# Performance work log

Measured on AMD Instinct MI355X. Metric: run time of the kernel, lower is better.

The kernel has to match this reference:

```python
import jax, jax.numpy as jnp
import numpy as np

N = 50000      # nodes
E = 800000     # edges (avg degree 16)
IN = 128       # in_feats
HID = 32       # hidden_feats per head
H = 4          # num_heads
NEG_SLOPE = 0.2


def setup_inputs() -> dict:
    key = jax.random.key(0)
    ks = jax.random.split(key, 13)
    x = jax.random.normal(ks[0], (N, IN), jnp.float32)
    src = jax.random.randint(ks[1], (E,), 0, N, jnp.int32)
    dst = jax.random.randint(ks[2], (E,), 0, N, jnp.int32)

    def lin(k, fi, fo):
        return jax.random.normal(k, (fi, fo), jnp.float32) * (1.0 / np.sqrt(fi))

    # conv1: IN -> H*HID
    W1 = lin(ks[3], IN, H * HID)
    al1 = jax.random.normal(ks[4], (H, HID), jnp.float32) * 0.1
    ar1 = jax.random.normal(ks[5], (H, HID), jnp.float32) * 0.1
    b1 = jnp.zeros((H, HID), jnp.float32)
    # conv2: H*HID -> H*HID
    W2 = lin(ks[6], H * HID, H * HID)
    al2 = jax.random.normal(ks[7], (H, HID), jnp.float32) * 0.1
    ar2 = jax.random.normal(ks[8], (H, HID), jnp.float32) * 0.1
    b2 = jnp.zeros((H, HID), jnp.float32)
    # fc: HID -> 1
    fcW = lin(ks[9], HID, 1)
    fcb = jnp.zeros((1,), jnp.float32)
    return {"x": x, "src": src, "dst": dst,
            "W1": W1, "al1": al1, "ar1": ar1, "b1": b1,
            "W2": W2, "al2": al2, "ar2": ar2, "b2": b2,
            "fcW": fcW, "fcb": fcb}


def gat_conv(x, src, dst, W, al, ar, b):
    # x: [N, F_in] -> feat: [N, H, HID]
    feat = (x @ W).reshape(N, H, HID)
    el = jnp.sum(feat * al, axis=-1)            # [N, H]
    er = jnp.sum(feat * ar, axis=-1)            # [N, H]
    e = jax.nn.leaky_relu(el[src] + er[dst], NEG_SLOPE)  # [E, H]
    # segment softmax over incoming edges of each dst node
    m = jax.ops.segment_max(e, dst, num_segments=N)      # [N, H]
    ex = jnp.exp(e - m[dst])                              # [E, H]
    denom = jax.ops.segment_sum(ex, dst, num_segments=N)  # [N, H]
    alpha = ex / denom[dst]                                # [E, H]
    msg = feat[src] * alpha[:, :, None]                    # [E, H, HID]
    out = jax.ops.segment_sum(msg, dst, num_segments=N)   # [N, H, HID]
    return out + b[None, :, :]


def reference(x, src, dst, W1, al1, ar1, b1, W2, al2, ar2, b2, fcW, fcb):
    h = gat_conv(x, src, dst, W1, al1, ar1, b1).reshape(N, H * HID)
    h = jax.nn.relu(h)
    # dropout(0.5) is identity in eval mode
    h = gat_conv(h, src, dst, W2, al2, ar2, b2).mean(axis=1)  # [N, HID]
    return h @ fcW + fcb                                       # [N, 1]
```

## Files before the change

### kernel.cpp

```cpp
#include <hip/hip_runtime.h>
#include <hip/hip_fp16.h>

#define LEAK 0.2f
#define CAP 64

static __device__ inline unsigned pack_h2(float a, float b) {
    __half2 h = __floats2half2_rn(a, b);
    unsigned u; __builtin_memcpy(&u, &h, 4); return u;
}
static __device__ inline float2 unpack_h2(unsigned u) {
    __half2 h; __builtin_memcpy(&h, &u, 4); return __half22float2(h);
}

__global__ __launch_bounds__(256) void k0(
    int* __restrict__ cnt, const float* __restrict__ W2,
    const float* __restrict__ al2, const float* __restrict__ ar2,
    const float* __restrict__ fcW, const float* __restrict__ b2,
    float* __restrict__ WfT, float* __restrict__ bc, int N, int zb) {
    const int t = threadIdx.x;
    int i = blockIdx.x * 256 + t;
    if (i < N) cnt[i] = 0;
    int fb = blockIdx.x - zb;
    if (fb >= 0) {
        int idx = fb * 256 + t;
        if (idx < 1536) {
            int c = idx >> 7, k = idx & 127;
            int h = c & 3, sel = c >> 2;
            const float* vec = (sel == 0) ? (al2 + 32 * h)
                             : (sel == 1) ? (ar2 + 32 * h) : fcW;
            float s = 0.f;
#pragma unroll 8
            for (int m = 0; m < 32; m++) s += W2[k * 128 + 32 * h + m] * vec[m];
            WfT[c * 128 + k] = s;
        } else if (idx < 1540) {
            int h = idx - 1536;
            float s = 0.f;
            for (int m = 0; m < 32; m++) s += b2[h * 32 + m] * fcW[m];
            bc[h] = s;
        }
    }
}

__global__ __launch_bounds__(256) void k_ell(
    const int* __restrict__ src, const int* __restrict__ dst,
    int* __restrict__ cnt, unsigned short* __restrict__ ell,
    int E, int N, int R) {
    const int part = blockIdx.x & 7;
    const int rank = blockIdx.x >> 3;
    const int S = (N + 7) >> 3;
    const int lo = part * S;
    const int hi = (lo + S < N) ? (lo + S) : N;
    const int per = (E + R - 1) / R;
    const int e0 = rank * per;
    const int e1 = (e0 + per < E) ? (e0 + per) : E;
    for (int e = e0 + threadIdx.x; e < e1; e += 256) {
        int d = dst[e];
        if (d >= lo && d < hi) {
            int s = src[e];
            int pos = atomicAdd(&cnt[d], 1);
            if (pos < CAP) ell[(size_t)d * CAP + pos] = (unsigned short)s;
        }
    }
}

__global__ __launch_bounds__(256, 4) void k_gemm(
    const float* __restrict__ X, const float* __restrict__ W,
    const float* __restrict__ al, const float* __restrict__ ar,
    float* __restrict__ el_nh, float* __restrict__ er_nh,
    uint2* __restrict__ fh2, int N) {
    __shared__ float sW[32 * 128];
    __shared__ float sXT[32 * 128];
    const int t = threadIdx.x;
    const int r0 = blockIdx.x * 128;
    const int tx = t & 15;
    const int ty = t >> 4;
    const float4* X4 = (const float4*)X;
    const float4* W4 = (const float4*)W;
    float4* sW4 = (float4*)sW;
    const float4* sXT4 = (const float4*)sXT;

    float4 acc[8][2];
#pragma unroll
    for (int r = 0; r < 8; r++) {
        acc[r][0] = make_float4(0.f, 0.f, 0.f, 0.f);
        acc[r][1] = make_float4(0.f, 0.f, 0.f, 0.f);
    }
    for (int ks = 0; ks < 4; ++ks) {
        if (ks) __syncthreads();
#pragma unroll
        for (int i = 0; i < 4; i++) {
            int idx = i * 256 + t;
            sW4[idx] = W4[1024 * ks + idx];
        }
#pragma unroll
        for (int i = 0; i < 4; i++) {
            int idx = i * 256 + t;
            int row = idx >> 3;
            int kq = idx & 7;
            float4 v = make_float4(0.f, 0.f, 0.f, 0.f);
            if (r0 + row < N) v = X4[(size_t)(r0 + row) * 32 + ks * 8 + kq];
            int sc = (((row >> 2) ^ kq)) * 4 + (row & 3);
            sXT[(4 * kq + 0) * 128 + sc] = v.x;
            sXT[(4 * kq + 1) * 128 + sc] = v.y;
            sXT[(4 * kq + 2) * 128 + sc] = v.z;
            sXT[(4 * kq + 3) * 128 + sc] = v.w;
        }
        __syncthreads();
#pragma unroll 4
        for (int k = 0; k < 32; k++) {
            float4 w0 = sW4[k * 32 + tx];
            float4 w1 = sW4[k * 32 + 16 + tx];
            float4 x0 = sXT4[k * 32 + (ty ^ (k >> 2))];
            float4 x1 = sXT4[k * 32 + ((16 + ty) ^ (k >> 2))];
            float xs[8] = {x0.x, x0.y, x0.z, x0.w, x1.x, x1.y, x1.z, x1.w};
#pragma unroll
            for (int r = 0; r < 8; r++) {
                acc[r][0].x += xs[r] * w0.x; acc[r][0].y += xs[r] * w0.y;
                acc[r][0].z += xs[r] * w0.z; acc[r][0].w += xs[r] * w0.w;
                acc[r][1].x += xs[r] * w1.x; acc[r][1].y += xs[r] * w1.y;
                acc[r][1].z += xs[r] * w1.z; acc[r][1].w += xs[r] * w1.w;
            }
        }
    }
    const float4* al4p = (const float4*)al;
    const float4* ar4p = (const float4*)ar;
    float4 alA = al4p[tx], alB = al4p[16 + tx];
    float4 arA = ar4p[tx], arB = ar4p[16 + tx];
#pragma unroll
    for (int r = 0; r < 8; r++) {
        int lrow = (r < 4) ? (ty * 4 + r) : (64 + ty * 4 + (r - 4));
        int row = r0 + lrow;
        bool ok = row < N;
        float4 a0 = acc[r][0], a1 = acc[r][1];
        if (ok) {
            uint2 d0, d1;
            d0.x = pack_h2(a0.x, a0.y); d0.y = pack_h2(a0.z, a0.w);
            d1.x = pack_h2(a1.x, a1.y); d1.y = pack_h2(a1.z, a1.w);
            fh2[(size_t)row * 32 + tx] = d0;
            fh2[(size_t)row * 32 + 16 + tx] = d1;
        }
        float elA = a0.x * alA.x + a0.y * alA.y + a0.z * alA.z + a0.w * alA.w;
        float erA = a0.x * arA.x + a0.y * arA.y + a0.z * arA.z + a0.w * arA.w;
        float elB = a1.x * alB.x + a1.y * alB.y + a1.z * alB.z + a1.w * alB.w;
        float erB = a1.x * arB.x + a1.y * arB.y + a1.z * arB.z + a1.w * arB.w;
#pragma unroll
        for (int off = 1; off < 8; off <<= 1) {
            elA += __shfl_xor(elA, off); erA += __shfl_xor(erA, off);
            elB += __shfl_xor(elB, off); erB += __shfl_xor(erB, off);
        }
        if (ok && tx == 0) {
            el_nh[row * 4 + 0] = elA; er_nh[row * 4 + 0] = erA;
            el_nh[row * 4 + 2] = elB; er_nh[row * 4 + 2] = erB;
        }
        if (ok && tx == 8) {
            el_nh[row * 4 + 1] = elA; er_nh[row * 4 + 1] = erA;
            el_nh[row * 4 + 3] = elB; er_nh[row * 4 + 3] = erB;
        }
    }
}

__global__ __launch_bounds__(256) void k_agg1P(
    const uint2* __restrict__ fh2, const float* __restrict__ el_nh,
    const float* __restrict__ er_nh, const unsigned short* __restrict__ ell,
    const int* __restrict__ cnt, const float* __restrict__ b1,
    const float* __restrict__ WfT, float2* __restrict__ Pag,
    float* __restrict__ er2, int N) {
    __shared__ float sWf[12 * 128];
    for (int i = threadIdx.x; i < 1536; i += 256) sWf[i] = WfT[i];
    __syncthreads();
    const int wave = threadIdx.x >> 6, lane = threadIdx.x & 63;
    const int nsub = lane >> 4, q = lane & 15, h = q >> 2;
    const int g = blockIdx.x * 4 + wave;
    const int n = g * 4 + nsub;
    const bool nok = n < N;
    const int nc = nok ? n : (N - 1);
    int deg = nok ? cnt[n] : 0; if (deg > CAP) deg = CAP;
    float er = nok ? er_nh[n * 4 + h] : 0.f;
    const unsigned short* row = ell + (size_t)nc * CAP;
    const uint4* fh4 = (const uint4*)fh2;

    int dm = deg;
    dm = max(dm, __shfl_xor(dm, 16));
    dm = max(dm, __shfl_xor(dm, 32));

    float acc[8] = {0.f, 0.f, 0.f, 0.f, 0.f, 0.f, 0.f, 0.f};
    float den = 0.f;
    for (int jt = 0; jt < dm; jt += 16) {
        int s_all = (jt + q < CAP) ? (int)row[jt + q] : 0;
        int lim = dm - jt; if (lim > 16) lim = 16;
        for (int u = 0; u < lim; u += 4) {
#pragma unroll
            for (int v = 0; v < 4; v++) {
                int jj = jt + u + v;
                bool valid = jj < deg;
                int s = __shfl(s_all, (lane & 48) | ((u + v) & 15));
                s = valid ? s : 0;
                float e = el_nh[s * 4 + h] + er;
                e = fmaxf(e, LEAK * e);
                float w = valid ? __expf(e) : 0.f;
                uint4 f = fh4[(size_t)s * 16 + q];
                float2 f0 = unpack_h2(f.x), f1 = unpack_h2(f.y);
                float2 f2 = unpack_h2(f.z), f3 = unpack_h2(f.w);
                acc[0] += w * f0.x; acc[1] += w * f0.y;
                acc[2] += w * f1.x; acc[3] += w * f1.y;
                acc[4] += w * f2.x; acc[5] += w * f2.y;
                acc[6] += w * f3.x; acc[7] += w * f3.y;
                den += w;
            }
        }
    }
    float inv = (den > 0.f) ? (1.f / den) : 0.f;
    float4 b1a = ((const float4*)b1)[q * 2];
    float4 b1b = ((const float4*)b1)[q * 2 + 1];
    float hv[8];
    hv[0] = fmaxf(acc[0] * inv + b1a.x, 0.f);
    hv[1] = fmaxf(acc[1] * inv + b1a.y, 0.f);
    hv[2] = fmaxf(acc[2] * inv + b1a.z, 0.f);
    hv[3] = fmaxf(acc[3] * inv + b1a.w, 0.f);
    hv[4] = fmaxf(acc[4] * inv + b1b.x, 0.f);
    hv[5] = fmaxf(acc[5] * inv + b1b.y, 0.f);
    hv[6] = fmaxf(acc[6] * inv + b1b.z, 0.f);
    hv[7] = fmaxf(acc[7] * inv + b1b.w, 0.f);
    float p[12];
#pragma unroll
    for (int c = 0; c < 12; c++) {
        const float* wr = sWf + c * 128 + q * 8;
        float4 wa = *(const float4*)wr;
        float4 wb = *(const float4*)(wr + 4);
        p[c] = hv[0] * wa.x + hv[1] * wa.y + hv[2] * wa.z + hv[3] * wa.w
             + hv[4] * wb.x + hv[5] * wb.y + hv[6] * wb.z + hv[7] * wb.w;
    }
#pragma unroll
    for (int off = 1; off < 16; off <<= 1) {
#pragma unroll
        for (int c = 0; c < 12; c++) p[c] += __shfl_xor(p[c], off);
    }
    if (nok) {
        if (q < 4) Pag[(size_t)n * 4 + q] = make_float2(p[q], p[8 + q]);
        else if (q < 8) er2[(size_t)n * 4 + (q - 4)] = p[q];
    }
}

__global__ __launch_bounds__(256) void k_agg2(const float2* __restrict__ Pag,
                                              const float* __restrict__ er2,
                                              const unsigned short* __restrict__ ell,
                                              const int* __restrict__ cnt,
                                              const float* __restrict__ bc,
                                              const float* __restrict__ fcb,
                                              float* __restrict__ out, int N) {
    int idx = blockIdx.x * 256 + threadIdx.x;
    int n = idx >> 2, h = idx & 3;
    if (n >= N) return;
    int deg = cnt[n]; if (deg > CAP) deg = CAP;
    float er = er2[(size_t)n * 4 + h];
    const unsigned short* row = ell + (size_t)n * CAP;
    float num = 0.f, den = 0.f;
    int j = 0, d4 = deg & ~3;
    for (; j < d4; j += 4) {
        ushort4 ss = *(const ushort4*)(row + j);
        int s0 = ss.x, s1 = ss.y, s2 = ss.z, s3 = ss.w;
        float2 g0 = Pag[(size_t)s0 * 4 + h];
        float2 g1 = Pag[(size_t)s1 * 4 + h];
        float2 g2 = Pag[(size_t)s2 * 4 + h];
        float2 g3 = Pag[(size_t)s3 * 4 + h];
        float e0 = g0.x + er; e0 = fmaxf(e0, LEAK * e0); float w0 = __expf(e0);
        float e1 = g1.x + er; e1 = fmaxf(e1, LEAK * e1); float w1 = __expf(e1);
        float e2 = g2.x + er; e2 = fmaxf(e2, LEAK * e2); float w2 = __expf(e2);
        float e3 = g3.x + er; e3 = fmaxf(e3, LEAK * e3); float w3 = __expf(e3);
        num += w0 * g0.y + w1 * g1.y + w2 * g2.y + w3 * g3.y;
        den += (w0 + w1) + (w2 + w3);
    }
    for (; j < deg; ++j) {
        int s = row[j];
        float2 gg = Pag[(size_t)s * 4 + h];
        float e = gg.x + er; e = fmaxf(e, LEAK * e);
        float w = __expf(e);
        num += w * gg.y; den += w;
    }
    float r = (den > 0.f) ? (num / den) : 0.f;
    r += bc[h];
    r += __shfl_xor(r, 1);
    r += __shfl_xor(r, 2);
    if (h == 0) out[n] = 0.25f * r + fcb[0];
}

extern "C" void kernel_launch(void* const* d_in, const int* in_sizes, int n_in,
                              void* d_out, int out_size, void* d_ws, size_t ws_size,
                              hipStream_t stream) {
    const float* x   = (const float*)d_in[0];
    const int* src   = (const int*)d_in[1];
    const int* dst   = (const int*)d_in[2];
    const float* W1  = (const float*)d_in[3];
    const float* al1 = (const float*)d_in[4];
    const float* ar1 = (const float*)d_in[5];
    const float* b1  = (const float*)d_in[6];
    const float* W2  = (const float*)d_in[7];
    const float* al2 = (const float*)d_in[8];
    const float* ar2 = (const float*)d_in[9];
    const float* b2  = (const float*)d_in[10];
    const float* fcW = (const float*)d_in[11];
    const float* fcb = (const float*)d_in[12];
    float* out = (float*)d_out;

    const int N = in_sizes[0] / 128;
    const int E = in_sizes[1];

    char* w = (char*)d_ws;
    size_t off = 0;
    auto alloc = [&](size_t bytes) {
        void* p = w + off;
        off = (off + bytes + 255) & ~(size_t)255;
        return p;
    };
    uint2* fh2   = (uint2*)alloc((size_t)N * 32 * 8);
    float* el_nh = (float*)alloc((size_t)N * 4 * 4);
    float* er_nh = (float*)alloc((size_t)N * 4 * 4);
    float2* Pag  = (float2*)alloc((size_t)N * 4 * 8);
    float* er2   = (float*)alloc((size_t)N * 4 * 4);
    float* WfT   = (float*)alloc((size_t)(12 * 128 + 4) * 4);
    float* bc    = WfT + 12 * 128;
    int* cnt     = (int*)alloc((size_t)N * 4);
    unsigned short* ell = (unsigned short*)alloc((size_t)N * CAP * 2);

    const int zb = (N + 255) / 256;
    const int ntiles = (N + 127) / 128;
    const int R = 256;
    const int aggB = (N + 15) / 16;

    k0<<<zb + 8, 256, 0, stream>>>(cnt, W2, al2, ar2, fcW, b2, WfT, bc, N, zb);
    k_ell<<<8 * R, 256, 0, stream>>>(src, dst, cnt, ell, E, N, R);
    k_gemm<<<ntiles, 256, 0, stream>>>(x, W1, al1, ar1, el_nh, er_nh, fh2, N);
    k_agg1P<<<aggB, 256, 0, stream>>>(fh2, el_nh, er_nh, ell, cnt, b1, WfT,
                                      Pag, er2, N);
    k_agg2<<<(N * 4 + 255) / 256, 256, 0, stream>>>(Pag, er2, ell, cnt, bc, fcb, out, N);
}
```

Measured before the change: 213.9 us.

## Merge init into GEMM and fuse both aggregations via cooperative grid sync

The counter-zeroing and weight-folding prologue now runs as extra blocks of the layer-1 GEMM kernel, which removes one launch. The two aggregation kernels are merged into one persistent cooperative kernel with grid-stride loops and a grid-wide sync between layer 1 and layer 2. If the cooperative launch fails, it falls back to two separate kernels. The shared-memory copy of the folded weights is padded and swizzled to reduce LDS bank conflicts. The persistent grid is capped at up to 8 blocks per CU, which may reduce latency hiding in the gather-heavy loops, and adds grid-sync and occupancy-query overhead.

```diff
diff --git a/kernel.cpp b/kernel.cpp
--- a/kernel.cpp
+++ b/kernel.cpp
@@ -1,8 +1,11 @@
 #include <hip/hip_runtime.h>
 #include <hip/hip_fp16.h>
+#include <hip/hip_cooperative_groups.h>
 
 #define LEAK 0.2f
 #define CAP 64
+
+namespace cg = cooperative_groups;
 
 static __device__ inline unsigned pack_h2(float a, float b) {
     __half2 h = __floats2half2_rn(a, b);
@@ -11,32 +14,136 @@
 static __device__ inline float2 unpack_h2(unsigned u) {
     __half2 h; __builtin_memcpy(&h, &u, 4); return __half22float2(h);
 }
-
-__global__ __launch_bounds__(256) void k0(
-    int* __restrict__ cnt, const float* __restrict__ W2,
-    const float* __restrict__ al2, const float* __restrict__ ar2,
-    const float* __restrict__ fcW, const float* __restrict__ b2,
-    float* __restrict__ WfT, float* __restrict__ bc, int N, int zb) {
+static __device__ inline int swz(int c, int j) {
+    int qb = j >> 3, r = j & 7;
+    return c * 144 + qb * 8 + (qb >> 2) * 4 + r;
+}
+
+__global__ __launch_bounds__(256, 4) void k1(
+    const float* __restrict__ X, const float* __restrict__ W,
+    const float* __restrict__ al, const float* __restrict__ ar,
+    float* __restrict__ el_nh, float* __restrict__ er_nh,
+    uint2* __restrict__ fh2,
+    int* __restrict__ cnt,
+    const float* __restrict__ W2, const float* __restrict__ al2,
+    const float* __restrict__ ar2, const float* __restrict__ fcW,
+    const float* __restrict__ b2, float* __restrict__ WfT,
+    float* __restrict__ bc, int N, int ntiles, int zb) {
+    __shared__ float sW[32 * 128];
+    __shared__ float sXT[32 * 128];
+    const int b = blockIdx.x;
     const int t = threadIdx.x;
-    int i = blockIdx.x * 256 + t;
-    if (i < N) cnt[i] = 0;
-    int fb = blockIdx.x - zb;
-    if (fb >= 0) {
-        int idx = fb * 256 + t;
-        if (idx < 1536) {
-            int c = idx >> 7, k = idx & 127;
-            int h = c & 3, sel = c >> 2;
-            const float* vec = (sel == 0) ? (al2 + 32 * h)
-                             : (sel == 1) ? (ar2 + 32 * h) : fcW;
-            float s = 0.f;
+
+    if (b >= ntiles) {
+        int bb = b - ntiles;
+        if (bb < zb) {
+            int i = bb * 256 + t;
+            if (i < N) cnt[i] = 0;
+        } else {
+            int idx = (bb - zb) * 256 + t;
+            if (idx < 1536) {
+                int c = idx >> 7, k = idx & 127;
+                int h = c & 3, sel = c >> 2;
+                const float* vec = (sel == 0) ? (al2 + 32 * h)
+                                 : (sel == 1) ? (ar2 + 32 * h) : fcW;
+                float s = 0.f;
 #pragma unroll 8
-            for (int m = 0; m < 32; m++) s += W2[k * 128 + 32 * h + m] * vec[m];
-            WfT[c * 128 + k] = s;
-        } else if (idx < 1540) {
-            int h = idx - 1536;
-            float s = 0.f;
-            for (int m = 0; m < 32; m++) s += b2[h * 32 + m] * fcW[m];
-            bc[h] = s;
+                for (int m = 0; m < 32; m++) s += W2[k * 128 + 32 * h + m] * vec[m];
+                WfT[c * 128 + k] = s;
+            } else if (idx < 1540) {
+                int h = idx - 1536;
+                float s = 0.f;
+                for (int m = 0; m < 32; m++) s += b2[h * 32 + m] * fcW[m];
+                bc[h] = s;
+            }
+        }
+        return;
+    }
+
+    const int r0 = b * 128;
+    const int tx = t & 15;
+    const int ty = t >> 4;
+    const float4* X4 = (const float4*)X;
+    const float4* W4 = (const float4*)W;
+    float4* sW4 = (float4*)sW;
+    const float4* sXT4 = (const float4*)sXT;
+
+    float4 acc[8][2];
+#pragma unroll
+    for (int r = 0; r < 8; r++) {
+        acc[r][0] = make_float4(0.f, 0.f, 0.f, 0.f);
+        acc[r][1] = make_float4(0.f, 0.f, 0.f, 0.f);
+    }
+    for (int ks = 0; ks < 4; ++ks) {
+        if (ks) __syncthreads();
+#pragma unroll
+        for (int i = 0; i < 4; i++) {
+            int idx = i * 256 + t;
+            sW4[idx] = W4[1024 * ks + idx];
+        }
+#pragma unroll
+        for (int i = 0; i < 4; i++) {
+            int idx = i * 256 + t;
+            int row = idx >> 3;
+            int kq = idx & 7;
+            float4 v = make_float4(0.f, 0.f, 0.f, 0.f);
+            if (r0 + row < N) v = X4[(size_t)(r0 + row) * 32 + ks * 8 + kq];
+            int sc = (((row >> 2) ^ kq)) * 4 + (row & 3);
+            sXT[(4 * kq + 0) * 128 + sc] = v.x;
+            sXT[(4 * kq + 1) * 128 + sc] = v.y;
+            sXT[(4 * kq + 2) * 128 + sc] = v.z;
+            sXT[(4 * kq + 3) * 128 + sc] = v.w;
+        }
+        __syncthreads();
+#pragma unroll 4
+        for (int k = 0; k < 32; k++) {
+            float4 w0 = sW4[k * 32 + tx];
+            float4 w1 = sW4[k * 32 + 16 + tx];
+            float4 x0 = sXT4[k * 32 + (ty ^ (k >> 2))];
+            float4 x1 = sXT4[k * 32 + ((16 + ty) ^ (k >> 2))];
+            float xs[8] = {x0.x, x0.y, x0.z, x0.w, x1.x, x1.y, x1.z, x1.w};
+#pragma unroll
+            for (int r = 0; r < 8; r++) {
+                acc[r][0].x += xs[r] * w0.x; acc[r][0].y += xs[r] * w0.y;
+                acc[r][0].z += xs[r] * w0.z; acc[r][0].w += xs[r] * w0.w;
+                acc[r][1].x += xs[r] * w1.x; acc[r][1].y += xs[r] * w1.y;
+                acc[r][1].z += xs[r] * w1.z; acc[r][1].w += xs[r] * w1.w;
+            }
+        }
+    }
+    const float4* al4p = (const float4*)al;
+    const float4* ar4p = (const float4*)ar;
+    float4 alA = al4p[tx], alB = al4p[16 + tx];
+    float4 arA = ar4p[tx], arB = ar4p[16 + tx];
+#pragma unroll
+    for (int r = 0; r < 8; r++) {
+        int lrow = (r < 4) ? (ty * 4 + r) : (64 + ty * 4 + (r - 4));
+        int row = r0 + lrow;
+        bool ok = row < N;
+        float4 a0 = acc[r][0], a1 = acc[r][1];
+        if (ok) {
+            uint2 d0, d1;
+            d0.x = pack_h2(a0.x, a0.y); d0.y = pack_h2(a0.z, a0.w);
+            d1.x = pack_h2(a1.x, a1.y); d1.y = pack_h2(a1.z, a1.w);
+            fh2[(size_t)row * 32 + tx] = d0;
+            fh2[(size_t)row * 32 + 16 + tx] = d1;
+        }
+        float elA = a0.x * alA.x + a0.y * alA.y + a0.z * alA.z + a0.w * alA.w;
+        float erA = a0.x * arA.x + a0.y * arA.y + a0.z * arA.z + a0.w * arA.w;
+        float elB = a1.x * alB.x + a1.y * alB.y + a1.z * alB.z + a1.w * alB.w;
+        float erB = a1.x * arB.x + a1.y * arB.y + a1.z * arB.z + a1.w * arB.w;
+#pragma unroll
+        for (int off = 1; off < 8; off <<= 1) {
+            elA += __shfl_xor(elA, off); erA += __shfl_xor(erA, off);
+            elB += __shfl_xor(elB, off); erB += __shfl_xor(erB, off);
+        }
+        if (ok && tx == 0) {
+            el_nh[row * 4 + 0] = elA; er_nh[row * 4 + 0] = erA;
+            el_nh[row * 4 + 2] = elB; er_nh[row * 4 + 2] = erB;
+        }
+        if (ok && tx == 8) {
+            el_nh[row * 4 + 1] = elA; er_nh[row * 4 + 1] = erA;
+            el_nh[row * 4 + 3] = elB; er_nh[row * 4 + 3] = erB;
         }
     }
 }
@@ -63,225 +170,170 @@
     }
 }
 
-__global__ __launch_bounds__(256, 4) void k_gemm(
-    const float* __restrict__ X, const float* __restrict__ W,
-    const float* __restrict__ al, const float* __restrict__ ar,
-    float* __restrict__ el_nh, float* __restrict__ er_nh,
-    uint2* __restrict__ fh2, int N) {
-    __shared__ float sW[32 * 128];
-    __shared__ float sXT[32 * 128];
-    const int t = threadIdx.x;
-    const int r0 = blockIdx.x * 128;
-    const int tx = t & 15;
-    const int ty = t >> 4;
-    const float4* X4 = (const float4*)X;
-    const float4* W4 = (const float4*)W;
-    float4* sW4 = (float4*)sW;
-    const float4* sXT4 = (const float4*)sXT;
-
-    float4 acc[8][2];
-#pragma unroll
-    for (int r = 0; r < 8; r++) {
-        acc[r][0] = make_float4(0.f, 0.f, 0.f, 0.f);
-        acc[r][1] = make_float4(0.f, 0.f, 0.f, 0.f);
-    }
-    for (int ks = 0; ks < 4; ++ks) {
-        if (ks) __syncthreads();
-#pragma unroll
-        for (int i = 0; i < 4; i++) {
-            int idx = i * 256 + t;
-            sW4[idx] = W4[1024 * ks + idx];
-        }
-#pragma unroll
-        for (int i = 0; i < 4; i++) {
-            int idx = i * 256 + t;
-            int row = idx >> 3;
-            int kq = idx & 7;
-            float4 v = make_float4(0.f, 0.f, 0.f, 0.f);
-            if (r0 + row < N) v = X4[(size_t)(r0 + row) * 32 + ks * 8 + kq];
-            int sc = (((row >> 2) ^ kq)) * 4 + (row & 3);
-            sXT[(4 * kq + 0) * 128 + sc] = v.x;
-            sXT[(4 * kq + 1) * 128 + sc] = v.y;
-            sXT[(4 * kq + 2) * 128 + sc] = v.z;
-            sXT[(4 * kq + 3) * 128 + sc] = v.w;
-        }
-        __syncthreads();
-#pragma unroll 4
-        for (int k = 0; k < 32; k++) {
-            float4 w0 = sW4[k * 32 + tx];
-            float4 w1 = sW4[k * 32 + 16 + tx];
-            float4 x0 = sXT4[k * 32 + (ty ^ (k >> 2))];
-            float4 x1 = sXT4[k * 32 + ((16 + ty) ^ (k >> 2))];
-            float xs[8] = {x0.x, x0.y, x0.z, x0.w, x1.x, x1.y, x1.z, x1.w};
-#pragma unroll
-            for (int r = 0; r < 8; r++) {
-                acc[r][0].x += xs[r] * w0.x; acc[r][0].y += xs[r] * w0.y;
-                acc[r][0].z += xs[r] * w0.z; acc[r][0].w += xs[r] * w0.w;
-                acc[r][1].x += xs[r] * w1.x; acc[r][1].y += xs[r] * w1.y;
-                acc[r][1].z += xs[r] * w1.z; acc[r][1].w += xs[r] * w1.w;
+static __device__ void agg1P_body(
+    const uint2* __restrict__ fh2, const float* __restrict__ el_nh,
+    const float* __restrict__ er_nh, const unsigned short* __restrict__ ell,
+    const int* __restrict__ cnt, const float* __restrict__ b1,
+    float2* __restrict__ Pag, float* __restrict__ er2, int N,
+    const float* sWf, int b, int nb, int t) {
+    const int wave = t >> 6, lane = t & 63;
+    const int nsub = lane >> 4, q = lane & 15, h = q >> 2;
+    const int ngroups = (N + 3) >> 2;
+    const uint4* fh4 = (const uint4*)fh2;
+    const int wbase = q * 8 + (q >> 2) * 4;
+
+    for (int g = b * 4 + wave; g < ngroups; g += nb * 4) {
+        const int n = g * 4 + nsub;
+        const bool nok = n < N;
+        const int nc = nok ? n : (N - 1);
+        int deg = nok ? cnt[n] : 0; if (deg > CAP) deg = CAP;
+        float er = nok ? er_nh[n * 4 + h] : 0.f;
+        const unsigned short* row = ell + (size_t)nc * CAP;
+
+        int dm = deg;
+        dm = max(dm, __shfl_xor(dm, 16));
+        dm = max(dm, __shfl_xor(dm, 32));
+
+        float acc[8] = {0.f, 0.f, 0.f, 0.f, 0.f, 0.f, 0.f, 0.f};
+        float den = 0.f;
+        for (int jt = 0; jt < dm; jt += 16) {
+            int s_all = (jt + q < CAP) ? (int)row[jt + q] : 0;
+            int lim = dm - jt; if (lim > 16) lim = 16;
+            for (int u = 0; u < lim; u += 4) {
+#pragma unroll
+                for (int v = 0; v < 4; v++) {
+                    int jj = jt + u + v;
+                    bool valid = jj < deg;
+                    int s = __shfl(s_all, (lane & 48) | ((u + v) & 15));
+                    s = valid ? s : 0;
+                    float e = el_nh[s * 4 + h] + er;
+                    e = fmaxf(e, LEAK * e);
+                    float w = valid ? __expf(e) : 0.f;
+                    uint4 f = fh4[(size_t)s * 16 + q];
+                    float2 f0 = unpack_h2(f.x), f1 = unpack_h2(f.y);
+                    float2 f2 = unpack_h2(f.z), f3 = unpack_h2(f.w);
+                    acc[0] += w * f0.x; acc[1] += w * f0.y;
+                    acc[2] += w * f1.x; acc[3] += w * f1.y;
+                    acc[4] += w * f2.x; acc[5] += w * f2.y;
+                    acc[6] += w * f3.x; acc[7] += w * f3.y;
+                    den += w;
+                }
             }
         }
-    }
-    const float4* al4p = (const float4*)al;
-    const float4* ar4p = (const float4*)ar;
-    float4 alA = al4p[tx], alB = al4p[16 + tx];
-    float4 arA = ar4p[tx], arB = ar4p[16 + tx];
-#pragma unroll
-    for (int r = 0; r < 8; r++) {
-        int lrow = (r < 4) ? (ty * 4 + r) : (64 + ty * 4 + (r - 4));
-        int row = r0 + lrow;
-        bool ok = row < N;
-        float4 a0 = acc[r][0], a1 = acc[r][1];
-        if (ok) {
-            uint2 d0, d1;
-            d0.x = pack_h2(a0.x, a0.y); d0.y = pack_h2(a0.z, a0.w);
-            d1.x = pack_h2(a1.x, a1.y); d1.y = pack_h2(a1.z, a1.w);
-            fh2[(size_t)row * 32 + tx] = d0;
-            fh2[(size_t)row * 32 + 16 + tx] = d1;
-        }
-        float elA = a0.x * alA.x + a0.y * alA.y + a0.z * alA.z + a0.w * alA.w;
-        float erA = a0.x * arA.x + a0.y * arA.y + a0.z * arA.z + a0.w * arA.w;
-        float elB = a1.x * alB.x + a1.y * alB.y + a1.z * alB.z + a1.w * alB.w;
-        float erB = a1.x * arB.x + a1.y * arB.y + a1.z * arB.z + a1.w * arB.w;
-#pragma unroll
-        for (int off = 1; off < 8; off <<= 1) {
-            elA += __shfl_xor(elA, off); erA += __shfl_xor(erA, off);
-            elB += __shfl_xor(elB, off); erB += __shfl_xor(erB, off);
-        }
-        if (ok && tx == 0) {
-            el_nh[row * 4 + 0] = elA; er_nh[row * 4 + 0] = erA;
-            el_nh[row * 4 + 2] = elB; er_nh[row * 4 + 2] = erB;
-        }
-        if (ok && tx == 8) {
-            el_nh[row * 4 + 1] = elA; er_nh[row * 4 + 1] = erA;
-            el_nh[row * 4 + 3] = elB; er_nh[row * 4 + 3] = erB;
-        }
-    }
-}
-
-__global__ __launch_bounds__(256) void k_agg1P(
+        float inv = (den > 0.f) ? (1.f / den) : 0.f;
+        float4 b1a = ((const float4*)b1)[q * 2];
+        float4 b1b = ((const float4*)b1)[q * 2 + 1];
+        float hv[8];
+        hv[0] = fmaxf(acc[0] * inv + b1a.x, 0.f);
+        hv[1] = fmaxf(acc[1] * inv + b1a.y, 0.f);
+        hv[2] = fmaxf(acc[2] * inv + b1a.z, 0.f);
+        hv[3] = fmaxf(acc[3] * inv + b1a.w, 0.f);
+        hv[4] = fmaxf(acc[4] * inv + b1b.x, 0.f);
+        hv[5] = fmaxf(acc[5] * inv + b1b.y, 0.f);
+        hv[6] = fmaxf(acc[6] * inv + b1b.z, 0.f);
+        hv[7] = fmaxf(acc[7] * inv + b1b.w, 0.f);
+        float p[12];
+#pragma unroll
+        for (int c = 0; c < 12; c++) {
+            const float* wr = sWf + c * 144 + wbase;
+            float4 wa = *(const float4*)wr;
+            float4 wb = *(const float4*)(wr + 4);
+            p[c] = hv[0] * wa.x + hv[1] * wa.y + hv[2] * wa.z + hv[3] * wa.w
+                 + hv[4] * wb.x + hv[5] * wb.y + hv[6] * wb.z + hv[7] * wb.w;
+        }
+#pragma unroll
+        for (int off = 1; off < 16; off <<= 1) {
+#pragma unroll
+            for (int c = 0; c < 12; c++) p[c] += __shfl_xor(p[c], off);
+        }
+        if (nok) {
+            if (q < 4) Pag[(size_t)n * 4 + q] = make_float2(p[q], p[8 + q]);
+            else if (q < 8) er2[(size_t)n * 4 + (q - 4)] = p[q];
+        }
+    }
+}
+
+static __device__ void agg2_body(
+    const float2* __restrict__ Pag, const float* __restrict__ er2,
+    const unsigned short* __restrict__ ell, const int* __restrict__ cnt,
+    const float* __restrict__ bc, const float* __restrict__ fcb,
+    float* __restrict__ out, int N, int b, int nb, int t) {
+    int total = N * 4;
+    for (int idx = b * 256 + t; idx < total; idx += nb * 256) {
+        int n = idx >> 2, h = idx & 3;
+        int deg = cnt[n]; if (deg > CAP) deg = CAP;
+        float er = er2[(size_t)n * 4 + h];
+        const unsigned short* row = ell + (size_t)n * CAP;
+        float num = 0.f, den = 0.f;
+        int j = 0, d4 = deg & ~3;
+        for (; j < d4; j += 4) {
+            ushort4 ss = *(const ushort4*)(row + j);
+            int s0 = ss.x, s1 = ss.y, s2 = ss.z, s3 = ss.w;
+            float2 g0 = Pag[(size_t)s0 * 4 + h];
+            float2 g1 = Pag[(size_t)s1 * 4 + h];
+            float2 g2 = Pag[(size_t)s2 * 4 + h];
+            float2 g3 = Pag[(size_t)s3 * 4 + h];
+            float e0 = g0.x + er; e0 = fmaxf(e0, LEAK * e0); float w0 = __expf(e0);
+            float e1 = g1.x + er; e1 = fmaxf(e1, LEAK * e1); float w1 = __expf(e1);
+            float e2 = g2.x + er; e2 = fmaxf(e2, LEAK * e2); float w2 = __expf(e2);
+            float e3 = g3.x + er; e3 = fmaxf(e3, LEAK * e3); float w3 = __expf(e3);
+            num += w0 * g0.y + w1 * g1.y + w2 * g2.y + w3 * g3.y;
+            den += (w0 + w1) + (w2 + w3);
+        }
+        for (; j < deg; ++j) {
+            int s = row[j];
+            float2 gg = Pag[(size_t)s * 4 + h];
+            float e = gg.x + er; e = fmaxf(e, LEAK * e);
+            float w = __expf(e);
+            num += w * gg.y; den += w;
+        }
+        float r = (den > 0.f) ? (num / den) : 0.f;
+        r += bc[h];
+        r += __shfl_xor(r, 1);
+        r += __shfl_xor(r, 2);
+        if (h == 0) out[n] = 0.25f * r + fcb[0];
+    }
+}
+
+__global__ __launch_bounds__(256) void k_aggC(
+    const uint2* __restrict__ fh2, const float* __restrict__ el_nh,
+    const float* __restrict__ er_nh, const unsigned short* __restrict__ ell,
+    const int* __restrict__ cnt, const float* __restrict__ b1,
+    const float* __restrict__ WfT, float2* __restrict__ Pag,
+    float* __restrict__ er2, const float* __restrict__ bc,
+    const float* __restrict__ fcb, float* __restrict__ out, int N) {
+    __shared__ float sWf[12 * 144];
+    for (int i = threadIdx.x; i < 1536; i += 256)
+        sWf[swz(i >> 7, i & 127)] = WfT[i];
+    __syncthreads();
+    cg::grid_group grid = cg::this_grid();
+    agg1P_body(fh2, el_nh, er_nh, ell, cnt, b1, Pag, er2, N,
+               sWf, blockIdx.x, gridDim.x, threadIdx.x);
+    grid.sync();
+    agg2_body(Pag, er2, ell, cnt, bc, fcb, out, N,
+              blockIdx.x, gridDim.x, threadIdx.x);
+}
+
+__global__ __launch_bounds__(256) void k_agg1P_f(
     const uint2* __restrict__ fh2, const float* __restrict__ el_nh,
     const float* __restrict__ er_nh, const unsigned short* __restrict__ ell,
     const int* __restrict__ cnt, const float* __restrict__ b1,
     const float* __restrict__ WfT, float2* __restrict__ Pag,
     float* __restrict__ er2, int N) {
-    __shared__ float sWf[12 * 128];
-    for (int i = threadIdx.x; i < 1536; i += 256) sWf[i] = WfT[i];
+    __shared__ float sWf[12 * 144];
+    for (int i = threadIdx.x; i < 1536; i += 256)
+        sWf[swz(i >> 7, i & 127)] = WfT[i];
     __syncthreads();
-    const int wave = threadIdx.x >> 6, lane = threadIdx.x & 63;
-    const int nsub = lane >> 4, q = lane & 15, h = q >> 2;
-    const int g = blockIdx.x * 4 + wave;
-    const int n = g * 4 + nsub;
-    const bool nok = n < N;
-    const int nc = nok ? n : (N - 1);
-    int deg = nok ? cnt[n] : 0; if (deg > CAP) deg = CAP;
-    float er = nok ? er_nh[n * 4 + h] : 0.f;
-    const unsigned short* row = ell + (size_t)nc * CAP;
-    const uint4* fh4 = (const uint4*)fh2;
-
-    int dm = deg;
-    dm = max(dm, __shfl_xor(dm, 16));
-    dm = max(dm, __shfl_xor(dm, 32));
-
-    float acc[8] = {0.f, 0.f, 0.f, 0.f, 0.f, 0.f, 0.f, 0.f};
-    float den = 0.f;
-    for (int jt = 0; jt < dm; jt += 16) {
-        int s_all = (jt + q < CAP) ? (int)row[jt + q] : 0;
-        int lim = dm - jt; if (lim > 16) lim = 16;
-        for (int u = 0; u < lim; u += 4) {
-#pragma unroll
-            for (int v = 0; v < 4; v++) {
-                int jj = jt + u + v;
-                bool valid = jj < deg;
-                int s = __shfl(s_all, (lane & 48) | ((u + v) & 15));
-                s = valid ? s : 0;
-                float e = el_nh[s * 4 + h] + er;
-                e = fmaxf(e, LEAK * e);
-                float w = valid ? __expf(e) : 0.f;
-                uint4 f = fh4[(size_t)s * 16 + q];
-                float2 f0 = unpack_h2(f.x), f1 = unpack_h2(f.y);
-                float2 f2 = unpack_h2(f.z), f3 = unpack_h2(f.w);
-                acc[0] += w * f0.x; acc[1] += w * f0.y;
-                acc[2] += w * f1.x; acc[3] += w * f1.y;
-                acc[4] += w * f2.x; acc[5] += w * f2.y;
-                acc[6] += w * f3.x; acc[7] += w * f3.y;
-                den += w;
-            }
-        }
-    }
-    float inv = (den > 0.f) ? (1.f / den) : 0.f;
-    float4 b1a = ((const float4*)b1)[q * 2];
-    float4 b1b = ((const float4*)b1)[q * 2 + 1];
-    float hv[8];
-    hv[0] = fmaxf(acc[0] * inv + b1a.x, 0.f);
-    hv[1] = fmaxf(acc[1] * inv + b1a.y, 0.f);
-    hv[2] = fmaxf(acc[2] * inv + b1a.z, 0.f);
-    hv[3] = fmaxf(acc[3] * inv + b1a.w, 0.f);
-    hv[4] = fmaxf(acc[4] * inv + b1b.x, 0.f);
-    hv[5] = fmaxf(acc[5] * inv + b1b.y, 0.f);
-    hv[6] = fmaxf(acc[6] * inv + b1b.z, 0.f);
-    hv[7] = fmaxf(acc[7] * inv + b1b.w, 0.f);
-    float p[12];
-#pragma unroll
-    for (int c = 0; c < 12; c++) {
-        const float* wr = sWf + c * 128 + q * 8;
-        float4 wa = *(const float4*)wr;
-        float4 wb = *(const float4*)(wr + 4);
-        p[c] = hv[0] * wa.x + hv[1] * wa.y + hv[2] * wa.z + hv[3] * wa.w
-             + hv[4] * wb.x + hv[5] * wb.y + hv[6] * wb.z + hv[7] * wb.w;
-    }
-#pragma unroll
-    for (int off = 1; off < 16; off <<= 1) {
-#pragma unroll
-        for (int c = 0; c < 12; c++) p[c] += __shfl_xor(p[c], off);
-    }
-    if (nok) {
-        if (q < 4) Pag[(size_t)n * 4 + q] = make_float2(p[q], p[8 + q]);
-        else if (q < 8) er2[(size_t)n * 4 + (q - 4)] = p[q];
-    }
-}
-
-__global__ __launch_bounds__(256) void k_agg2(const float2* __restrict__ Pag,
-                                              const float* __restrict__ er2,
-                                              const unsigned short* __restrict__ ell,
-                                              const int* __restrict__ cnt,
-                                              const float* __restrict__ bc,
-                                              const float* __restrict__ fcb,
-                                              float* __restrict__ out, int N) {
-    int idx = blockIdx.x * 256 + threadIdx.x;
-    int n = idx >> 2, h = idx & 3;
-    if (n >= N) return;
-    int deg = cnt[n]; if (deg > CAP) deg = CAP;
-    float er = er2[(size_t)n * 4 + h];
-    const unsigned short* row = ell + (size_t)n * CAP;
-    float num = 0.f, den = 0.f;
-    int j = 0, d4 = deg & ~3;
-    for (; j < d4; j += 4) {
-        ushort4 ss = *(const ushort4*)(row + j);
-        int s0 = ss.x, s1 = ss.y, s2 = ss.z, s3 = ss.w;
-        float2 g0 = Pag[(size_t)s0 * 4 + h];
-        float2 g1 = Pag[(size_t)s1 * 4 + h];
-        float2 g2 = Pag[(size_t)s2 * 4 + h];
-        float2 g3 = Pag[(size_t)s3 * 4 + h];
-        float e0 = g0.x + er; e0 = fmaxf(e0, LEAK * e0); float w0 = __expf(e0);
-        float e1 = g1.x + er; e1 = fmaxf(e1, LEAK * e1); float w1 = __expf(e1);
-        float e2 = g2.x + er; e2 = fmaxf(e2, LEAK * e2); float w2 = __expf(e2);
-        float e3 = g3.x + er; e3 = fmaxf(e3, LEAK * e3); float w3 = __expf(e3);
-        num += w0 * g0.y + w1 * g1.y + w2 * g2.y + w3 * g3.y;
-        den += (w0 + w1) + (w2 + w3);
-    }
-    for (; j < deg; ++j) {
-        int s = row[j];
-        float2 gg = Pag[(size_t)s * 4 + h];
-        float e = gg.x + er; e = fmaxf(e, LEAK * e);
-        float w = __expf(e);
-        num += w * gg.y; den += w;
-    }
-    float r = (den > 0.f) ? (num / den) : 0.f;
-    r += bc[h];
-    r += __shfl_xor(r, 1);
-    r += __shfl_xor(r, 2);
-    if (h == 0) out[n] = 0.25f * r + fcb[0];
+    agg1P_body(fh2, el_nh, er_nh, ell, cnt, b1, Pag, er2, N,
+               sWf, blockIdx.x, gridDim.x, threadIdx.x);
+}
+__global__ __launch_bounds__(256) void k_agg2_f(
+    const float2* __restrict__ Pag, const float* __restrict__ er2,
+    const unsigned short* __restrict__ ell, const int* __restrict__ cnt,
+    const float* __restrict__ bc, const float* __restrict__ fcb,
+    float* __restrict__ out, int N) {
+    agg2_body(Pag, er2, ell, cnt, bc, fcb, out, N,
+              blockIdx.x, gridDim.x, threadIdx.x);
 }
 
 extern "C" void kernel_launch(void* const* d_in, const int* in_sizes, int n_in,
@@ -325,12 +377,30 @@
     const int zb = (N + 255) / 256;
     const int ntiles = (N + 127) / 128;
     const int R = 256;
-    const int aggB = (N + 15) / 16;
-
-    k0<<<zb + 8, 256, 0, stream>>>(cnt, W2, al2, ar2, fcW, b2, WfT, bc, N, zb);
+
+    k1<<<ntiles + zb + 8, 256, 0, stream>>>(
+        x, W1, al1, ar1, el_nh, er_nh, fh2,
+        cnt, W2, al2, ar2, fcW, b2, WfT, bc, N, ntiles, zb);
     k_ell<<<8 * R, 256, 0, stream>>>(src, dst, cnt, ell, E, N, R);
-    k_gemm<<<ntiles, 256, 0, stream>>>(x, W1, al1, ar1, el_nh, er_nh, fh2, N);
-    k_agg1P<<<aggB, 256, 0, stream>>>(fh2, el_nh, er_nh, ell, cnt, b1, WfT,
-                                      Pag, er2, N);
-    k_agg2<<<(N * 4 + 255) / 256, 256, 0, stream>>>(Pag, er2, ell, cnt, bc, fcb, out, N);
-}
+
+    hipError_t lerr = hipErrorUnknown;
+    int per_cu = 0;
+    hipError_t qerr = hipOccupancyMaxActiveBlocksPerMultiprocessor(
+        &per_cu, (const void*)k_aggC, 256, 0);
+    if (qerr == hipSuccess && per_cu >= 1) {
+        if (per_cu > 8) per_cu = 8;
+        int grid = per_cu * 256;
+        void* params[] = {
+            (void*)&fh2, (void*)&el_nh, (void*)&er_nh, (void*)&ell,
+            (void*)&cnt, (void*)&b1, (void*)&WfT, (void*)&Pag,
+            (void*)&er2, (void*)&bc, (void*)&fcb, (void*)&out, (void*)&N};
+        lerr = hipLaunchCooperativeKernel((const void*)k_aggC, dim3(grid),
+                                          dim3(256), params, 0, stream);
+    }
+    if (lerr != hipSuccess) {
+        k_agg1P_f<<<(N + 15) / 16, 256, 0, stream>>>(
+            fh2, el_nh, er_nh, ell, cnt, b1, WfT, Pag, er2, N);
+        k_agg2_f<<<(N * 4 + 255) / 256, 256, 0, stream>>>(
+            Pag, er2, ell, cnt, bc, fcb, out, N);
+    }
+}
```

Result: slower. 296.1 us (+38.4%).

## Fuse layer-1 GEMM into prep kernel, batch gathers in agg1, pad shared weights

Applied to the files above, without the earlier changes.

Merges the layer-1 GEMM with the count-zeroing and weight-folding prep into one launch, cutting one kernel launch. The GEMM tiles run in the leading blocks and the prep work in the trailing blocks. In the layer-1 aggregation, the per-edge loop now issues eight el and feature gathers up front before consuming them, to raise memory-level parallelism. The shared folded-weight table is padded and swizzled to avoid LDS bank conflicts. The batched gathers raise register pressure, and the fused kernel's 4-blocks-per-SM launch bound now also applies to the trivial prep blocks.

```diff
diff --git a/kernel.cpp b/kernel.cpp
--- a/kernel.cpp
+++ b/kernel.cpp
@@ -11,32 +11,136 @@
 static __device__ inline float2 unpack_h2(unsigned u) {
     __half2 h; __builtin_memcpy(&h, &u, 4); return __half22float2(h);
 }
-
-__global__ __launch_bounds__(256) void k0(
-    int* __restrict__ cnt, const float* __restrict__ W2,
-    const float* __restrict__ al2, const float* __restrict__ ar2,
-    const float* __restrict__ fcW, const float* __restrict__ b2,
-    float* __restrict__ WfT, float* __restrict__ bc, int N, int zb) {
+static __device__ inline int swz(int c, int j) {
+    int qb = j >> 3, r = j & 7;
+    return c * 144 + qb * 8 + (qb >> 2) * 4 + r;
+}
+
+__global__ __launch_bounds__(256, 4) void k1(
+    const float* __restrict__ X, const float* __restrict__ W,
+    const float* __restrict__ al, const float* __restrict__ ar,
+    float* __restrict__ el_nh, float* __restrict__ er_nh,
+    uint2* __restrict__ fh2,
+    int* __restrict__ cnt,
+    const float* __restrict__ W2, const float* __restrict__ al2,
+    const float* __restrict__ ar2, const float* __restrict__ fcW,
+    const float* __restrict__ b2, float* __restrict__ WfT,
+    float* __restrict__ bc, int N, int ntiles, int zb) {
+    __shared__ float sW[32 * 128];
+    __shared__ float sXT[32 * 128];
+    const int b = blockIdx.x;
     const int t = threadIdx.x;
-    int i = blockIdx.x * 256 + t;
-    if (i < N) cnt[i] = 0;
-    int fb = blockIdx.x - zb;
-    if (fb >= 0) {
-        int idx = fb * 256 + t;
-        if (idx < 1536) {
-            int c = idx >> 7, k = idx & 127;
-            int h = c & 3, sel = c >> 2;
-            const float* vec = (sel == 0) ? (al2 + 32 * h)
-                             : (sel == 1) ? (ar2 + 32 * h) : fcW;
-            float s = 0.f;
+
+    if (b >= ntiles) {
+        int bb = b - ntiles;
+        if (bb < zb) {
+            int i = bb * 256 + t;
+            if (i < N) cnt[i] = 0;
+        } else {
+            int idx = (bb - zb) * 256 + t;
+            if (idx < 1536) {
+                int c = idx >> 7, k = idx & 127;
+                int h = c & 3, sel = c >> 2;
+                const float* vec = (sel == 0) ? (al2 + 32 * h)
+                                 : (sel == 1) ? (ar2 + 32 * h) : fcW;
+                float s = 0.f;
 #pragma unroll 8
-            for (int m = 0; m < 32; m++) s += W2[k * 128 + 32 * h + m] * vec[m];
-            WfT[c * 128 + k] = s;
-        } else if (idx < 1540) {
-            int h = idx - 1536;
-            float s = 0.f;
-            for (int m = 0; m < 32; m++) s += b2[h * 32 + m] * fcW[m];
-            bc[h] = s;
+                for (int m = 0; m < 32; m++) s += W2[k * 128 + 32 * h + m] * vec[m];
+                WfT[c * 128 + k] = s;
+            } else if (idx < 1540) {
+                int h = idx - 1536;
+                float s = 0.f;
+                for (int m = 0; m < 32; m++) s += b2[h * 32 + m] * fcW[m];
+                bc[h] = s;
+            }
+        }
+        return;
+    }
+
+    const int r0 = b * 128;
+    const int tx = t & 15;
+    const int ty = t >> 4;
+    const float4* X4 = (const float4*)X;
+    const float4* W4 = (const float4*)W;
+    float4* sW4 = (float4*)sW;
+    const float4* sXT4 = (const float4*)sXT;
+
+    float4 acc[8][2];
+#pragma unroll
+    for (int r = 0; r < 8; r++) {
+        acc[r][0] = make_float4(0.f, 0.f, 0.f, 0.f);
+        acc[r][1] = make_float4(0.f, 0.f, 0.f, 0.f);
+    }
+    for (int ks = 0; ks < 4; ++ks) {
+        if (ks) __syncthreads();
+#pragma unroll
+        for (int i = 0; i < 4; i++) {
+            int idx = i * 256 + t;
+            sW4[idx] = W4[1024 * ks + idx];
+        }
+#pragma unroll
+        for (int i = 0; i < 4; i++) {
+            int idx = i * 256 + t;
+            int row = idx >> 3;
+            int kq = idx & 7;
+            float4 v = make_float4(0.f, 0.f, 0.f, 0.f);
+            if (r0 + row < N) v = X4[(size_t)(r0 + row) * 32 + ks * 8 + kq];
+            int sc = (((row >> 2) ^ kq)) * 4 + (row & 3);
+            sXT[(4 * kq + 0) * 128 + sc] = v.x;
+            sXT[(4 * kq + 1) * 128 + sc] = v.y;
+            sXT[(4 * kq + 2) * 128 + sc] = v.z;
+            sXT[(4 * kq + 3) * 128 + sc] = v.w;
+        }
+        __syncthreads();
+#pragma unroll 4
+        for (int k = 0; k < 32; k++) {
+            float4 w0 = sW4[k * 32 + tx];
+            float4 w1 = sW4[k * 32 + 16 + tx];
+            float4 x0 = sXT4[k * 32 + (ty ^ (k >> 2))];
+            float4 x1 = sXT4[k * 32 + ((16 + ty) ^ (k >> 2))];
+            float xs[8] = {x0.x, x0.y, x0.z, x0.w, x1.x, x1.y, x1.z, x1.w};
+#pragma unroll
+            for (int r = 0; r < 8; r++) {
+                acc[r][0].x += xs[r] * w0.x; acc[r][0].y += xs[r] * w0.y;
+                acc[r][0].z += xs[r] * w0.z; acc[r][0].w += xs[r] * w0.w;
+                acc[r][1].x += xs[r] * w1.x; acc[r][1].y += xs[r] * w1.y;
+                acc[r][1].z += xs[r] * w1.z; acc[r][1].w += xs[r] * w1.w;
+            }
+        }
+    }
+    const float4* al4p = (const float4*)al;
+    const float4* ar4p = (const float4*)ar;
+    float4 alA = al4p[tx], alB = al4p[16 + tx];
+    float4 arA = ar4p[tx], arB = ar4p[16 + tx];
+#pragma unroll
+    for (int r = 0; r < 8; r++) {
+        int lrow = (r < 4) ? (ty * 4 + r) : (64 + ty * 4 + (r - 4));
+        int row = r0 + lrow;
+        bool ok = row < N;
+        float4 a0 = acc[r][0], a1 = acc[r][1];
+        if (ok) {
+            uint2 d0, d1;
+            d0.x = pack_h2(a0.x, a0.y); d0.y = pack_h2(a0.z, a0.w);
+            d1.x = pack_h2(a1.x, a1.y); d1.y = pack_h2(a1.z, a1.w);
+            fh2[(size_t)row * 32 + tx] = d0;
+            fh2[(size_t)row * 32 + 16 + tx] = d1;
+        }
+        float elA = a0.x * alA.x + a0.y * alA.y + a0.z * alA.z + a0.w * alA.w;
+        float erA = a0.x * arA.x + a0.y * arA.y + a0.z * arA.z + a0.w * arA.w;
+        float elB = a1.x * alB.x + a1.y * alB.y + a1.z * alB.z + a1.w * alB.w;
+        float erB = a1.x * arB.x + a1.y * arB.y + a1.z * arB.z + a1.w * arB.w;
+#pragma unroll
+        for (int off = 1; off < 8; off <<= 1) {
+            elA += __shfl_xor(elA, off); erA += __shfl_xor(erA, off);
+            elB += __shfl_xor(elB, off); erB += __shfl_xor(erB, off);
+        }
+        if (ok && tx == 0) {
+            el_nh[row * 4 + 0] = elA; er_nh[row * 4 + 0] = erA;
+            el_nh[row * 4 + 2] = elB; er_nh[row * 4 + 2] = erB;
+        }
+        if (ok && tx == 8) {
+            el_nh[row * 4 + 1] = elA; er_nh[row * 4 + 1] = erA;
+            el_nh[row * 4 + 3] = elB; er_nh[row * 4 + 3] = erB;
         }
     }
 }
@@ -63,121 +167,27 @@
     }
 }
 
-__global__ __launch_bounds__(256, 4) void k_gemm(
-    const float* __restrict__ X, const float* __restrict__ W,
-    const float* __restrict__ al, const float* __restrict__ ar,
-    float* __restrict__ el_nh, float* __restrict__ er_nh,
-    uint2* __restrict__ fh2, int N) {
-    __shared__ float sW[32 * 128];
-    __shared__ float sXT[32 * 128];
-    const int t = threadIdx.x;
-    const int r0 = blockIdx.x * 128;
-    const int tx = t & 15;
-    const int ty = t >> 4;
-    const float4* X4 = (const float4*)X;
-    const float4* W4 = (const float4*)W;
-    float4* sW4 = (float4*)sW;
-    const float4* sXT4 = (const float4*)sXT;
-
-    float4 acc[8][2];
-#pragma unroll
-    for (int r = 0; r < 8; r++) {
-        acc[r][0] = make_float4(0.f, 0.f, 0.f, 0.f);
-        acc[r][1] = make_float4(0.f, 0.f, 0.f, 0.f);
-    }
-    for (int ks = 0; ks < 4; ++ks) {
-        if (ks) __syncthreads();
-#pragma unroll
-        for (int i = 0; i < 4; i++) {
-            int idx = i * 256 + t;
-            sW4[idx] = W4[1024 * ks + idx];
-        }
-#pragma unroll
-        for (int i = 0; i < 4; i++) {
-            int idx = i * 256 + t;
-            int row = idx >> 3;
-            int kq = idx & 7;
-            float4 v = make_float4(0.f, 0.f, 0.f, 0.f);
-            if (r0 + row < N) v = X4[(size_t)(r0 + row) * 32 + ks * 8 + kq];
-            int sc = (((row >> 2) ^ kq)) * 4 + (row & 3);
-            sXT[(4 * kq + 0) * 128 + sc] = v.x;
-            sXT[(4 * kq + 1) * 128 + sc] = v.y;
-            sXT[(4 * kq + 2) * 128 + sc] = v.z;
-            sXT[(4 * kq + 3) * 128 + sc] = v.w;
-        }
-        __syncthreads();
-#pragma unroll 4
-        for (int k = 0; k < 32; k++) {
-            float4 w0 = sW4[k * 32 + tx];
-            float4 w1 = sW4[k * 32 + 16 + tx];
-            float4 x0 = sXT4[k * 32 + (ty ^ (k >> 2))];
-            float4 x1 = sXT4[k * 32 + ((16 + ty) ^ (k >> 2))];
-            float xs[8] = {x0.x, x0.y, x0.z, x0.w, x1.x, x1.y, x1.z, x1.w};
-#pragma unroll
-            for (int r = 0; r < 8; r++) {
-                acc[r][0].x += xs[r] * w0.x; acc[r][0].y += xs[r] * w0.y;
-                acc[r][0].z += xs[r] * w0.z; acc[r][0].w += xs[r] * w0.w;
-                acc[r][1].x += xs[r] * w1.x; acc[r][1].y += xs[r] * w1.y;
-                acc[r][1].z += xs[r] * w1.z; acc[r][1].w += xs[r] * w1.w;
-            }
-        }
-    }
-    const float4* al4p = (const float4*)al;
-    const float4* ar4p = (const float4*)ar;
-    float4 alA = al4p[tx], alB = al4p[16 + tx];
-    float4 arA = ar4p[tx], arB = ar4p[16 + tx];
-#pragma unroll
-    for (int r = 0; r < 8; r++) {
-        int lrow = (r < 4) ? (ty * 4 + r) : (64 + ty * 4 + (r - 4));
-        int row = r0 + lrow;
-        bool ok = row < N;
-        float4 a0 = acc[r][0], a1 = acc[r][1];
-        if (ok) {
-            uint2 d0, d1;
-            d0.x = pack_h2(a0.x, a0.y); d0.y = pack_h2(a0.z, a0.w);
-            d1.x = pack_h2(a1.x, a1.y); d1.y = pack_h2(a1.z, a1.w);
-            fh2[(size_t)row * 32 + tx] = d0;
-            fh2[(size_t)row * 32 + 16 + tx] = d1;
-        }
-        float elA = a0.x * alA.x + a0.y * alA.y + a0.z * alA.z + a0.w * alA.w;
-        float erA = a0.x * arA.x + a0.y * arA.y + a0.z * arA.z + a0.w * arA.w;
-        float elB = a1.x * alB.x + a1.y * alB.y + a1.z * alB.z + a1.w * alB.w;
-        float erB = a1.x * arB.x + a1.y * arB.y + a1.z * arB.z + a1.w * arB.w;
-#pragma unroll
-        for (int off = 1; off < 8; off <<= 1) {
-            elA += __shfl_xor(elA, off); erA += __shfl_xor(erA, off);
-            elB += __shfl_xor(elB, off); erB += __shfl_xor(erB, off);
-        }
-        if (ok && tx == 0) {
-            el_nh[row * 4 + 0] = elA; er_nh[row * 4 + 0] = erA;
-            el_nh[row * 4 + 2] = elB; er_nh[row * 4 + 2] = erB;
-        }
-        if (ok && tx == 8) {
-            el_nh[row * 4 + 1] = elA; er_nh[row * 4 + 1] = erA;
-            el_nh[row * 4 + 3] = elB; er_nh[row * 4 + 3] = erB;
-        }
-    }
-}
-
 __global__ __launch_bounds__(256) void k_agg1P(
     const uint2* __restrict__ fh2, const float* __restrict__ el_nh,
     const float* __restrict__ er_nh, const unsigned short* __restrict__ ell,
     const int* __restrict__ cnt, const float* __restrict__ b1,
     const float* __restrict__ WfT, float2* __restrict__ Pag,
     float* __restrict__ er2, int N) {
-    __shared__ float sWf[12 * 128];
-    for (int i = threadIdx.x; i < 1536; i += 256) sWf[i] = WfT[i];
+    __shared__ float sWf[12 * 144];
+    for (int i = threadIdx.x; i < 1536; i += 256)
+        sWf[swz(i >> 7, i & 127)] = WfT[i];
     __syncthreads();
     const int wave = threadIdx.x >> 6, lane = threadIdx.x & 63;
     const int nsub = lane >> 4, q = lane & 15, h = q >> 2;
-    const int g = blockIdx.x * 4 + wave;
-    const int n = g * 4 + nsub;
+    const int wbase = q * 8 + (q >> 2) * 4;
+    const uint4* fh4 = (const uint4*)fh2;
+
+    const int n = blockIdx.x * 16 + wave * 4 + nsub;
     const bool nok = n < N;
     const int nc = nok ? n : (N - 1);
     int deg = nok ? cnt[n] : 0; if (deg > CAP) deg = CAP;
     float er = nok ? er_nh[n * 4 + h] : 0.f;
     const unsigned short* row = ell + (size_t)nc * CAP;
-    const uint4* fh4 = (const uint4*)fh2;
 
     int dm = deg;
     dm = max(dm, __shfl_xor(dm, 16));
@@ -188,19 +198,29 @@
     for (int jt = 0; jt < dm; jt += 16) {
         int s_all = (jt + q < CAP) ? (int)row[jt + q] : 0;
         int lim = dm - jt; if (lim > 16) lim = 16;
-        for (int u = 0; u < lim; u += 4) {
-#pragma unroll
-            for (int v = 0; v < 4; v++) {
+        for (int u = 0; u < lim; u += 8) {
+            int sv[8]; float ev[8]; uint4 fv[8];
+#pragma unroll
+            for (int v = 0; v < 8; v++) {
                 int jj = jt + u + v;
                 bool valid = jj < deg;
                 int s = __shfl(s_all, (lane & 48) | ((u + v) & 15));
-                s = valid ? s : 0;
-                float e = el_nh[s * 4 + h] + er;
+                sv[v] = valid ? s : 0;
+                sv[v] = (jj < dm) ? sv[v] : 0;
+            }
+#pragma unroll
+            for (int v = 0; v < 8; v++) ev[v] = el_nh[sv[v] * 4 + h];
+#pragma unroll
+            for (int v = 0; v < 8; v++) fv[v] = fh4[(size_t)sv[v] * 16 + q];
+#pragma unroll
+            for (int v = 0; v < 8; v++) {
+                int jj = jt + u + v;
+                bool valid = jj < deg;
+                float e = ev[v] + er;
                 e = fmaxf(e, LEAK * e);
                 float w = valid ? __expf(e) : 0.f;
-                uint4 f = fh4[(size_t)s * 16 + q];
-                float2 f0 = unpack_h2(f.x), f1 = unpack_h2(f.y);
-                float2 f2 = unpack_h2(f.z), f3 = unpack_h2(f.w);
+                float2 f0 = unpack_h2(fv[v].x), f1 = unpack_h2(fv[v].y);
+                float2 f2 = unpack_h2(fv[v].z), f3 = unpack_h2(fv[v].w);
                 acc[0] += w * f0.x; acc[1] += w * f0.y;
                 acc[2] += w * f1.x; acc[3] += w * f1.y;
                 acc[4] += w * f2.x; acc[5] += w * f2.y;
@@ -224,7 +244,7 @@
     float p[12];
 #pragma unroll
     for (int c = 0; c < 12; c++) {
-        const float* wr = sWf + c * 128 + q * 8;
+        const float* wr = sWf + c * 144 + wbase;
         float4 wa = *(const float4*)wr;
         float4 wb = *(const float4*)(wr + 4);
         p[c] = hv[0] * wa.x + hv[1] * wa.y + hv[2] * wa.z + hv[3] * wa.w
@@ -241,13 +261,11 @@
     }
 }
 
-__global__ __launch_bounds__(256) void k_agg2(const float2* __restrict__ Pag,
-                                              const float* __restrict__ er2,
-                                              const unsigned short* __restrict__ ell,
-                                              const int* __restrict__ cnt,
-                                              const float* __restrict__ bc,
-                                              const float* __restrict__ fcb,
-                                              float* __restrict__ out, int N) {
+__global__ __launch_bounds__(256) void k_agg2(
+    const float2* __restrict__ Pag, const float* __restrict__ er2,
+    const unsigned short* __restrict__ ell, const int* __restrict__ cnt,
+    const float* __restrict__ bc, const float* __restrict__ fcb,
+    float* __restrict__ out, int N) {
     int idx = blockIdx.x * 256 + threadIdx.x;
     int n = idx >> 2, h = idx & 3;
     if (n >= N) return;
@@ -325,12 +343,13 @@
     const int zb = (N + 255) / 256;
     const int ntiles = (N + 127) / 128;
     const int R = 256;
-    const int aggB = (N + 15) / 16;
-
-    k0<<<zb + 8, 256, 0, stream>>>(cnt, W2, al2, ar2, fcW, b2, WfT, bc, N, zb);
+
+    k1<<<ntiles + zb + 8, 256, 0, stream>>>(
+        x, W1, al1, ar1, el_nh, er_nh, fh2,
+        cnt, W2, al2, ar2, fcW, b2, WfT, bc, N, ntiles, zb);
     k_ell<<<8 * R, 256, 0, stream>>>(src, dst, cnt, ell, E, N, R);
-    k_gemm<<<ntiles, 256, 0, stream>>>(x, W1, al1, ar1, el_nh, er_nh, fh2, N);
-    k_agg1P<<<aggB, 256, 0, stream>>>(fh2, el_nh, er_nh, ell, cnt, b1, WfT,
-                                      Pag, er2, N);
-    k_agg2<<<(N * 4 + 255) / 256, 256, 0, stream>>>(Pag, er2, ell, cnt, bc, fcb, out, N);
-}
+    k_agg1P<<<(N + 15) / 16, 256, 0, stream>>>(
+        fh2, el_nh, er_nh, ell, cnt, b1, WfT, Pag, er2, N);
+    k_agg2<<<(N * 4 + 255) / 256, 256, 0, stream>>>(
+        Pag, er2, ell, cnt, bc, fcb, out, N);
+}
```

After: 205.5 us. 1.04x faster.
